# Kernel optimization log

Measured on AMD Instinct MI355X. Metric: run time of the kernel, lower is better.

The kernel has to match this reference:

```python
import jax, jax.numpy as jnp
import numpy as np

D_MODEL = 1024
N_HEADS = 16
D_K = D_MODEL // N_HEADS


def setup_inputs() -> dict:
    key = jax.random.key(0)
    ks = jax.random.split(key, 10)
    s = 1.0 / np.sqrt(D_MODEL)
    def lin(k):
        kw, kb = jax.random.split(k)
        W = jax.random.uniform(kw, (D_MODEL, D_MODEL), jnp.float32, -s, s)
        b = jax.random.uniform(kb, (D_MODEL,), jnp.float32, -s, s)
        return W, b
    Wq, bq = lin(ks[0])
    Wk, bk = lin(ks[1])
    Wv, bv = lin(ks[2])
    Wo, bo = lin(ks[3])
    x = jax.random.normal(ks[4], (2, 2048, D_MODEL), jnp.float32)
    gamma = jnp.ones((D_MODEL,), jnp.float32)
    beta = jnp.zeros((D_MODEL,), jnp.float32)
    return {"x": x, "Wq": Wq, "bq": bq, "Wk": Wk, "bk": bk,
            "Wv": Wv, "bv": bv, "Wo": Wo, "bo": bo,
            "gamma": gamma, "beta": beta}


def _mha(x, Wq, bq, Wk, bk, Wv, bv, Wo, bo, gamma, beta):
    B, S, _ = x.shape
    residual = x
    # Linear uses y = x @ W.T + b (torch nn.Linear convention)
    q = (x @ Wq.T + bq).reshape(B, S, N_HEADS, D_K).transpose(0, 2, 1, 3)
    k = (x @ Wk.T + bk).reshape(B, S, N_HEADS, D_K).transpose(0, 2, 1, 3)
    v = (x @ Wv.T + bv).reshape(B, S, N_HEADS, D_K).transpose(0, 2, 1, 3)
    scores = jnp.einsum("bhqd,bhkd->bhqk", q, k) / jnp.sqrt(jnp.float32(D_K))
    attn = jax.nn.softmax(scores, axis=-1)
    out = jnp.einsum("bhqk,bhkd->bhqd", attn, v)
    out = out.transpose(0, 2, 1, 3).reshape(B, S, D_MODEL)
    out = out @ Wo.T + bo
    h = out + residual
    mu = jnp.mean(h, axis=-1, keepdims=True)
    var = jnp.var(h, axis=-1, keepdims=True)
    h = (h - mu) / jnp.sqrt(var + 1e-5) * gamma + beta
    return jnp.where(h >= 0, h, 0.01 * h)


def reference(x, Wq, bq, Wk, bk, Wv, bv, Wo, bo, gamma, beta):
    return _mha(x, Wq, bq, Wk, bk, Wv, bv, Wo, bo, gamma, beta)
```

## Files before the change

kernel.cpp:

```cpp
#include <hip/hip_runtime.h>

#define DM   1024
#define NH   16
#define DK   64
#define SEQ  2048
#define BATCH 2

typedef __attribute__((ext_vector_type(8))) short bf16x8;
typedef __attribute__((ext_vector_type(4))) float f32x4;
typedef __attribute__((ext_vector_type(16))) float f32x16;

__device__ __forceinline__ unsigned short f2bf(float f) {
    unsigned int u = __builtin_bit_cast(unsigned int, f);
    u += 0x7FFFu + ((u >> 16) & 1u);
    return (unsigned short)(u >> 16);
}

__global__ __launch_bounds__(256)
void cvt_kernel(const float* __restrict__ x,
                const float* __restrict__ wq, const float* __restrict__ wk,
                const float* __restrict__ wv, const float* __restrict__ wo,
                unsigned short* __restrict__ xb,
                unsigned short* __restrict__ wqkvb,
                unsigned short* __restrict__ wob)
{
    const int seg = blockIdx.y;
    const float* src;
    unsigned short* dst;
    int n;
    if (seg == 0)      { src = x;  dst = xb;                  n = 4 << 20; }
    else if (seg == 1) { src = wq; dst = wqkvb;               n = 1 << 20; }
    else if (seg == 2) { src = wk; dst = wqkvb + (1 << 20);   n = 1 << 20; }
    else if (seg == 3) { src = wv; dst = wqkvb + (2 << 20);   n = 1 << 20; }
    else               { src = wo; dst = wob;                 n = 1 << 20; }
    for (int i = (blockIdx.x * 256 + threadIdx.x) * 4; i < n; i += 1024 * 256 * 4) {
        const float4 v = *reinterpret_cast<const float4*>(&src[i]);
        ushort4 o;
        o.x = f2bf(v.x); o.y = f2bf(v.y); o.z = f2bf(v.z); o.w = f2bf(v.w);
        *reinterpret_cast<ushort4*>(&dst[i]) = o;
    }
}

template <int MODE, int BN>
__global__ __launch_bounds__(256)
void gemm2_kernel(const unsigned short* __restrict__ Ab,
                  const unsigned short* __restrict__ Wall,
                  const float* __restrict__ B0, const float* __restrict__ B1,
                  const float* __restrict__ B2,
                  unsigned short* __restrict__ q_ws,
                  unsigned short* __restrict__ k_ws,
                  unsigned short* __restrict__ vt_ws,
                  const float* __restrict__ resid,
                  float* __restrict__ h_ws)
{
    __shared__ unsigned short sA[128 * 32];
    __shared__ unsigned short sB[BN * 32];

    const int tid = threadIdx.x, lane = tid & 63, wid = tid >> 6;
    const int n0 = blockIdx.x * BN, m0 = blockIdx.y * 128;
    const int z  = (MODE == 0) ? blockIdx.z : 0;
    const unsigned short* W = Wall + (size_t)z * (1 << 20);
    const float* bias = (MODE == 0) ? (z == 0 ? B0 : (z == 1 ? B1 : B2)) : B0;

    const int g = lane >> 4, lq = lane & 15;
    const int wr = wid >> 1, wc = wid & 1;
    const int rA = lane >> 2;
    const int csh = (lane & 3) * 8;

    f32x4 acc[4][BN / 32] = {};

    for (int k0 = 0; k0 < DM; k0 += 32) {
        #pragma unroll
        for (int i = 0; i < 2; ++i) {
            const int c = wid * 2 + i;
            __builtin_amdgcn_global_load_lds(
                (const __attribute__((address_space(1))) unsigned int*)
                    &Ab[(size_t)(m0 + c * 16 + rA) * DM + k0 + csh],
                (__attribute__((address_space(3))) unsigned int*)&sA[c * 512],
                16, 0, 0);
        }
        #pragma unroll
        for (int i = 0; i < BN / 64; ++i) {
            const int c = wid * (BN / 64) + i;
            __builtin_amdgcn_global_load_lds(
                (const __attribute__((address_space(1))) unsigned int*)
                    &W[(size_t)(n0 + c * 16 + rA) * DM + k0 + csh],
                (__attribute__((address_space(3))) unsigned int*)&sB[c * 512],
                16, 0, 0);
        }
        __syncthreads();

        bf16x8 a[4], b[BN / 32];
        #pragma unroll
        for (int m = 0; m < 4; ++m)
            a[m] = *reinterpret_cast<const bf16x8*>(&sA[(wr * 64 + m * 16 + lq) * 32 + 8 * g]);
        #pragma unroll
        for (int n = 0; n < BN / 32; ++n)
            b[n] = *reinterpret_cast<const bf16x8*>(&sB[(wc * (BN / 2) + n * 16 + lq) * 32 + 8 * g]);
        #pragma unroll
        for (int m = 0; m < 4; ++m)
            #pragma unroll
            for (int n = 0; n < BN / 32; ++n)
                acc[m][n] = __builtin_amdgcn_mfma_f32_16x16x32_bf16(
                    a[m], b[n], acc[m][n], 0, 0, 0);
        __syncthreads();
    }

    #pragma unroll
    for (int m = 0; m < 4; ++m) {
        #pragma unroll
        for (int n = 0; n < BN / 32; ++n) {
            #pragma unroll
            for (int j = 0; j < 4; ++j) {
                const int row = m0 + wr * 64 + m * 16 + 4 * g + j;
                const int col = n0 + wc * (BN / 2) + n * 16 + lq;
                float v = acc[m][n][j] + bias[col];
                if constexpr (MODE == 0) {
                    const int b_ = row >> 11, s = row & (SEQ - 1);
                    const int hh = col >> 6,  d = col & (DK - 1);
                    if (z == 0)
                        q_ws[(((size_t)(b_ * NH + hh) * SEQ + s) << 6) + d] = f2bf(v * 0.18033688f);
                    else if (z == 1)
                        k_ws[(((size_t)(b_ * NH + hh) * SEQ + s) << 6) + d] = f2bf(v);
                    else
                        vt_ws[((size_t)(b_ * NH + hh) * DK + d) * SEQ + s] = f2bf(v);
                } else {
                    const size_t idx = (size_t)row * DM + col;
                    h_ws[idx] = v + resid[idx];
                }
            }
        }
    }
}

__global__ __launch_bounds__(512)
void attn_kernel(const unsigned short* __restrict__ q_ws,
                 const unsigned short* __restrict__ k_ws,
                 const unsigned short* __restrict__ vt_ws,
                 unsigned short* __restrict__ ao_ws)
{
    __shared__ unsigned short lds4[8][4096];

    const int tid = threadIdx.x;
    const int lane = tid & 63, wid = tid >> 6;
    const int s = wid >> 2, w4 = wid & 3;
    const int l31 = lane & 31, h = lane >> 5;
    const int bh = blockIdx.y;
    const int q0 = blockIdx.x * 128;
    const int q  = q0 + w4 * 32 + l31;

    const size_t qbase = ((size_t)bh * SEQ + q) * DK;
    bf16x8 qf[4];
    #pragma unroll
    for (int j = 0; j < 4; ++j)
        qf[j] = *reinterpret_cast<const bf16x8*>(&q_ws[qbase + j * 16 + h * 8]);

    const short one_bf = (short)0x3F80;
    const bf16x8 onesf = {one_bf, one_bf, one_bf, one_bf, one_bf, one_bf, one_bf, one_bf};

    const int l8 = lane >> 3, l7 = lane & 7;
    const int scol = 8 * (l7 ^ l8);
    const unsigned short* kp0 = &k_ws [((size_t)bh * SEQ + s * 1024 + w4 * 16 + l8) * DK + scol];
    const unsigned short* kp1 = kp0 + 8 * DK;
    const unsigned short* vp0 = &vt_ws[((size_t)bh * DK + w4 * 16 + l8) * SEQ + s * 1024 + scol];
    const unsigned short* vp1 = vp0 + 8 * SEQ;

    const int r7 = l31 & 7;
    const unsigned short* pK[4];
    const unsigned short* pV[4];
    #pragma unroll
    for (int j = 0; j < 4; ++j) {
        const int ck = 8 * (((j << 1) + h) ^ r7);
        pK[j] = &lds4[2 * s][l31 * 64 + ck];
        pV[j] = &lds4[4 + 2 * s][l31 * 64 + ck];
    }

    f32x16 oacc[2] = {};
    f32x16 lacc = {};

    const int dst0 = w4 * 2 * 512, dst1 = (w4 * 2 + 1) * 512;

    auto stage = [&](int b) {
        __builtin_amdgcn_global_load_lds(
            (const __attribute__((address_space(1))) unsigned int*)kp0,
            (__attribute__((address_space(3))) unsigned int*)&lds4[2 * s + b][dst0], 16, 0, 0);
        __builtin_amdgcn_global_load_lds(
            (const __attribute__((address_space(1))) unsigned int*)kp1,
            (__attribute__((address_space(3))) unsigned int*)&lds4[2 * s + b][dst1], 16, 0, 0);
        __builtin_amdgcn_global_load_lds(
            (const __attribute__((address_space(1))) unsigned int*)vp0,
            (__attribute__((address_space(3))) unsigned int*)&lds4[4 + 2 * s + b][dst0], 16, 0, 0);
        __builtin_amdgcn_global_load_lds(
            (const __attribute__((address_space(1))) unsigned int*)vp1,
            (__attribute__((address_space(3))) unsigned int*)&lds4[4 + 2 * s + b][dst1], 16, 0, 0);
        kp0 += 64 * DK; kp1 += 64 * DK;
        vp0 += 64;      vp1 += 64;
    };

    auto compute = [&](int OFF) {
        f32x16 st0 = {}, st1 = {};
        __builtin_amdgcn_s_setprio(1);
        #pragma unroll
        for (int j = 0; j < 4; ++j) {
            const bf16x8 k0 = *reinterpret_cast<const bf16x8*>(pK[j] + OFF);
            const bf16x8 k1 = *reinterpret_cast<const bf16x8*>(pK[j] + OFF + 2048);
            st0 = __builtin_amdgcn_mfma_f32_32x32x16_bf16(k0, qf[j], st0, 0, 0, 0);
            st1 = __builtin_amdgcn_mfma_f32_32x32x16_bf16(k1, qf[j], st1, 0, 0, 0);
        }
        __builtin_amdgcn_s_setprio(0);

        bf16x8 pb[4];
        #pragma unroll
        for (int ss = 0; ss < 2; ++ss) {
            #pragma unroll
            for (int jg = 0; jg < 2; ++jg) {
                const int rb = 8 * jg;
                float e0, e1, e2, e3, e4, e5, e6, e7;
                #define EXP2(dst, src) asm("v_exp_f32 %0, %1" : "=v"(dst) : "v"(src))
                if (ss == 0) {
                    EXP2(e0, st0[rb + 0]); EXP2(e1, st0[rb + 1]);
                    EXP2(e2, st0[rb + 2]); EXP2(e3, st0[rb + 3]);
                    EXP2(e4, st0[rb + 4]); EXP2(e5, st0[rb + 5]);
                    EXP2(e6, st0[rb + 6]); EXP2(e7, st0[rb + 7]);
                } else {
                    EXP2(e0, st1[rb + 0]); EXP2(e1, st1[rb + 1]);
                    EXP2(e2, st1[rb + 2]); EXP2(e3, st1[rb + 3]);
                    EXP2(e4, st1[rb + 4]); EXP2(e5, st1[rb + 5]);
                    EXP2(e6, st1[rb + 6]); EXP2(e7, st1[rb + 7]);
                }
                #undef EXP2
                unsigned int wA, wB, wC, wD;
                asm("v_cvt_pk_bf16_f32 %0, %1, %2" : "=v"(wA) : "v"(e0), "v"(e1));
                asm("v_cvt_pk_bf16_f32 %0, %1, %2" : "=v"(wB) : "v"(e2), "v"(e3));
                asm("v_cvt_pk_bf16_f32 %0, %1, %2" : "=v"(wC) : "v"(e4), "v"(e5));
                asm("v_cvt_pk_bf16_f32 %0, %1, %2" : "=v"(wD) : "v"(e6), "v"(e7));
                asm("v_permlane32_swap_b32 %0, %1" : "+v"(wA), "+v"(wC));
                asm("v_permlane32_swap_b32 %0, %1" : "+v"(wB), "+v"(wD));
                uint4 ww;
                ww.x = wA; ww.y = wB; ww.z = wC; ww.w = wD;
                pb[2 * ss + jg] = __builtin_bit_cast(bf16x8, ww);
            }
        }

        __builtin_amdgcn_s_setprio(1);
        #pragma unroll
        for (int jg = 0; jg < 4; ++jg)
            lacc = __builtin_amdgcn_mfma_f32_32x32x16_bf16(onesf, pb[jg], lacc, 0, 0, 0);
        #pragma unroll
        for (int dt = 0; dt < 2; ++dt)
            #pragma unroll
            for (int jg = 0; jg < 4; ++jg) {
                const bf16x8 vv = *reinterpret_cast<const bf16x8*>(pV[jg] + OFF + dt * 2048);
                oacc[dt] = __builtin_amdgcn_mfma_f32_32x32x16_bf16(vv, pb[jg], oacc[dt], 0, 0, 0);
            }
        __builtin_amdgcn_s_setprio(0);
    };

    stage(0);
    __syncthreads();
    #pragma unroll 1
    for (int tt = 0; tt < 8; ++tt) {
        stage(1);
        compute(0);
        __syncthreads();
        if (tt < 7) stage(0);
        compute(4096);
        __syncthreads();
    }

    float* fl = (float*)&lds4[0][0];
    if (s == 1) {
        float* p = fl + (size_t)(w4 * 64 + lane) * 33;
        #pragma unroll
        for (int dt = 0; dt < 2; ++dt)
            #pragma unroll
            for (int r = 0; r < 16; ++r) p[dt * 16 + r] = oacc[dt][r];
        p[32] = lacc[0];
    }
    __syncthreads();
    if (s == 0) {
        const float* p = fl + (size_t)(w4 * 64 + lane) * 33;
        #pragma unroll
        for (int dt = 0; dt < 2; ++dt)
            #pragma unroll
            for (int r = 0; r < 16; ++r) oacc[dt][r] += p[dt * 16 + r];
        const float rl = 1.0f / (lacc[0] + p[32]);

        const int b_ = bh >> 4, hh = bh & 15;
        unsigned short* aop = &ao_ws[(size_t)(b_ * SEQ + q) * DM + hh * 64];
        #pragma unroll
        for (int dt = 0; dt < 2; ++dt) {
            #pragma unroll
            for (int qd = 0; qd < 4; ++qd) {
                ushort4 o;
                o.x = f2bf(oacc[dt][4 * qd + 0] * rl);
                o.y = f2bf(oacc[dt][4 * qd + 1] * rl);
                o.z = f2bf(oacc[dt][4 * qd + 2] * rl);
                o.w = f2bf(oacc[dt][4 * qd + 3] * rl);
                *reinterpret_cast<ushort4*>(&aop[dt * 32 + 8 * qd + 4 * h]) = o;
            }
        }
    }
}

__global__ __launch_bounds__(256)
void ln_kernel(const float* __restrict__ h, const float* __restrict__ gamma,
               const float* __restrict__ beta, float* __restrict__ out)
{
    __shared__ float s1[4], s2[4];
    const int row = blockIdx.x, tid = threadIdx.x;
    const float4 v = reinterpret_cast<const float4*>(h + (size_t)row * DM)[tid];
    float sum = v.x + v.y + v.z + v.w;
    float sq  = v.x * v.x + v.y * v.y + v.z * v.z + v.w * v.w;
    #pragma unroll
    for (int mk = 1; mk <= 32; mk <<= 1) {
        sum += __shfl_xor(sum, mk);
        sq  += __shfl_xor(sq, mk);
    }
    if ((tid & 63) == 0) { s1[tid >> 6] = sum; s2[tid >> 6] = sq; }
    __syncthreads();
    sum = s1[0] + s1[1] + s1[2] + s1[3];
    sq  = s2[0] + s2[1] + s2[2] + s2[3];
    const float mu = sum * (1.f / DM);
    const float var = sq * (1.f / DM) - mu * mu;
    const float rstd = rsqrtf(var + 1e-5f);
    const float4 gv = reinterpret_cast<const float4*>(gamma)[tid];
    const float4 bv = reinterpret_cast<const float4*>(beta)[tid];
    float4 o;
    o.x = (v.x - mu) * rstd * gv.x + bv.x;
    o.y = (v.y - mu) * rstd * gv.y + bv.y;
    o.z = (v.z - mu) * rstd * gv.z + bv.z;
    o.w = (v.w - mu) * rstd * gv.w + bv.w;
    o.x = o.x >= 0.f ? o.x : 0.01f * o.x;
    o.y = o.y >= 0.f ? o.y : 0.01f * o.y;
    o.z = o.z >= 0.f ? o.z : 0.01f * o.z;
    o.w = o.w >= 0.f ? o.w : 0.01f * o.w;
    reinterpret_cast<float4*>(out + (size_t)row * DM)[tid] = o;
}

extern "C" void kernel_launch(void* const* d_in, const int* in_sizes, int n_in,
                              void* d_out, int out_size, void* d_ws, size_t ws_size,
                              hipStream_t stream)
{
    const float* x     = (const float*)d_in[0];
    const float* Wq    = (const float*)d_in[1];
    const float* bq    = (const float*)d_in[2];
    const float* Wk    = (const float*)d_in[3];
    const float* bk    = (const float*)d_in[4];
    const float* Wv    = (const float*)d_in[5];
    const float* bv    = (const float*)d_in[6];
    const float* Wo    = (const float*)d_in[7];
    const float* bo    = (const float*)d_in[8];
    const float* gamma = (const float*)d_in[9];
    const float* beta  = (const float*)d_in[10];

    char* ws = (char*)d_ws;
    unsigned short* q_ws   = (unsigned short*)(ws);
    unsigned short* k_ws   = (unsigned short*)(ws + (8u << 20));
    unsigned short* vt_ws  = (unsigned short*)(ws + (16u << 20));
    unsigned short* ao_ws  = (unsigned short*)(ws + (24u << 20));
    unsigned short* xb_ws  = (unsigned short*)(ws + (32u << 20));
    unsigned short* wqkv_b = (unsigned short*)(ws + (40u << 20));
    unsigned short* wo_b   = (unsigned short*)(ws + (46u << 20));
    float* h_ws = (float*)ws;

    const dim3 blk(256);
    cvt_kernel<<<dim3(1024, 5), blk, 0, stream>>>(
        x, Wq, Wk, Wv, Wo, xb_ws, wqkv_b, wo_b);
    gemm2_kernel<0, 128><<<dim3(8, 32, 3), blk, 0, stream>>>(
        xb_ws, wqkv_b, bq, bk, bv, q_ws, k_ws, vt_ws, nullptr, nullptr);
    attn_kernel<<<dim3(16, 32), dim3(512), 0, stream>>>(q_ws, k_ws, vt_ws, ao_ws);
    gemm2_kernel<1, 64><<<dim3(16, 32, 1), blk, 0, stream>>>(
        ao_ws, wo_b, bo, nullptr, nullptr, nullptr, nullptr, nullptr, x, h_ws);
    ln_kernel<<<dim3(4096), blk, 0, stream>>>(h_ws, gamma, beta, (float*)d_out);
}
```

Baseline: 129.8 us.

## Double GEMM K-tile to 64 with XOR-swizzled LDS; remap attention blocks per XCD

The projection GEMM now stages 64-wide K slices instead of 32, halving the number of barrier-separated iterations. It also applies an XOR swizzle to the LDS column layout so the MFMA fragment reads avoid bank conflicts. Separately, the attention kernel remaps the linear block id so that all query tiles of a given batch-head land on the same XCD, improving L2 reuse of K/V. The cost is twice the LDS per GEMM block, which may lower occupancy.

```diff
diff --git a/kernel.cpp b/kernel.cpp
--- a/kernel.cpp
+++ b/kernel.cpp
@@ -53,8 +53,8 @@
                   const float* __restrict__ resid,
                   float* __restrict__ h_ws)
 {
-    __shared__ unsigned short sA[128 * 32];
-    __shared__ unsigned short sB[BN * 32];
+    __shared__ unsigned short sA[128 * 64];
+    __shared__ unsigned short sB[BN * 64];
 
     const int tid = threadIdx.x, lane = tid & 63, wid = tid >> 6;
     const int n0 = blockIdx.x * BN, m0 = blockIdx.y * 128;
@@ -64,45 +64,56 @@
 
     const int g = lane >> 4, lq = lane & 15;
     const int wr = wid >> 1, wc = wid & 1;
-    const int rA = lane >> 2;
-    const int csh = (lane & 3) * 8;
+    const int l8 = lane >> 3, l7 = lane & 7;
+    const int scol = 8 * (l7 ^ l8);
+
+    const int r7 = lq & 7;
 
     f32x4 acc[4][BN / 32] = {};
 
-    for (int k0 = 0; k0 < DM; k0 += 32) {
-        #pragma unroll
-        for (int i = 0; i < 2; ++i) {
-            const int c = wid * 2 + i;
+    for (int k0 = 0; k0 < DM; k0 += 64) {
+        #pragma unroll
+        for (int i = 0; i < 4; ++i) {
+            const int c = wid * 4 + i;
             __builtin_amdgcn_global_load_lds(
                 (const __attribute__((address_space(1))) unsigned int*)
-                    &Ab[(size_t)(m0 + c * 16 + rA) * DM + k0 + csh],
+                    &Ab[(size_t)(m0 + c * 8 + l8) * DM + k0 + scol],
                 (__attribute__((address_space(3))) unsigned int*)&sA[c * 512],
                 16, 0, 0);
         }
         #pragma unroll
-        for (int i = 0; i < BN / 64; ++i) {
-            const int c = wid * (BN / 64) + i;
+        for (int i = 0; i < BN / 32; ++i) {
+            const int c = wid * (BN / 32) + i;
             __builtin_amdgcn_global_load_lds(
                 (const __attribute__((address_space(1))) unsigned int*)
-                    &W[(size_t)(n0 + c * 16 + rA) * DM + k0 + csh],
+                    &W[(size_t)(n0 + c * 8 + l8) * DM + k0 + scol],
                 (__attribute__((address_space(3))) unsigned int*)&sB[c * 512],
                 16, 0, 0);
         }
         __syncthreads();
 
-        bf16x8 a[4], b[BN / 32];
-        #pragma unroll
-        for (int m = 0; m < 4; ++m)
-            a[m] = *reinterpret_cast<const bf16x8*>(&sA[(wr * 64 + m * 16 + lq) * 32 + 8 * g]);
-        #pragma unroll
-        for (int n = 0; n < BN / 32; ++n)
-            b[n] = *reinterpret_cast<const bf16x8*>(&sB[(wc * (BN / 2) + n * 16 + lq) * 32 + 8 * g]);
-        #pragma unroll
-        for (int m = 0; m < 4; ++m)
-            #pragma unroll
-            for (int n = 0; n < BN / 32; ++n)
-                acc[m][n] = __builtin_amdgcn_mfma_f32_16x16x32_bf16(
-                    a[m], b[n], acc[m][n], 0, 0, 0);
+        #pragma unroll
+        for (int kk = 0; kk < 2; ++kk) {
+            bf16x8 a[4], b[BN / 32];
+            #pragma unroll
+            for (int m = 0; m < 4; ++m) {
+                const int row = wr * 64 + m * 16 + lq;
+                a[m] = *reinterpret_cast<const bf16x8*>(
+                    &sA[row * 64 + 8 * ((4 * kk + g) ^ r7)]);
+            }
+            #pragma unroll
+            for (int n = 0; n < BN / 32; ++n) {
+                const int row = wc * (BN / 2) + n * 16 + lq;
+                b[n] = *reinterpret_cast<const bf16x8*>(
+                    &sB[row * 64 + 8 * ((4 * kk + g) ^ r7)]);
+            }
+            #pragma unroll
+            for (int m = 0; m < 4; ++m)
+                #pragma unroll
+                for (int n = 0; n < BN / 32; ++n)
+                    acc[m][n] = __builtin_amdgcn_mfma_f32_16x16x32_bf16(
+                        a[m], b[n], acc[m][n], 0, 0, 0);
+        }
         __syncthreads();
     }
 
@@ -145,9 +156,12 @@
     const int lane = tid & 63, wid = tid >> 6;
     const int s = wid >> 2, w4 = wid & 3;
     const int l31 = lane & 31, h = lane >> 5;
-    const int bh = blockIdx.y;
-    const int q0 = blockIdx.x * 128;
-    const int q  = q0 + w4 * 32 + l31;
+
+    const int bid  = blockIdx.x + 16 * blockIdx.y;
+    const int xcd  = bid & 7, slot = bid >> 3;
+    const int bh   = 4 * xcd + (slot >> 4);
+    const int q0   = (slot & 15) * 128;
+    const int q    = q0 + w4 * 32 + l31;
 
     const size_t qbase = ((size_t)bh * SEQ + q) * DK;
     bf16x8 qf[4];
```

After: 135.7 us. 1.05x slower.
